# Performance work log

Measured on AMD Instinct MI355X. Metric: run time of the kernel, lower is better.

The kernel has to match this reference:

```python
import jax, jax.numpy as jnp
import numpy as np

N_NODES = 50000
N_EDGES = 800000
HIDDEN = 128
HEADS = 4
LAYERS = 2
NEG_SLOPE = 0.2


def setup_inputs() -> dict:
    key = jax.random.key(0)
    ks = jax.random.split(key, 12)
    s_in = 1.0 / np.sqrt(HIDDEN)
    x = jax.random.normal(ks[0], (N_NODES, HIDDEN), dtype=jnp.float32)
    edge_index = jax.random.randint(ks[1], (2, N_EDGES), 0, N_NODES, dtype=jnp.int64)
    conv_w = jax.random.normal(ks[2], (LAYERS, HIDDEN, HEADS * HIDDEN), dtype=jnp.float32) * s_in
    att_src = jax.random.normal(ks[3], (LAYERS, HEADS, HIDDEN), dtype=jnp.float32) * s_in
    att_dst = jax.random.normal(ks[4], (LAYERS, HEADS, HIDDEN), dtype=jnp.float32) * s_in
    conv_b = jax.random.normal(ks[5], (LAYERS, HIDDEN), dtype=jnp.float32) * 0.01
    proj_w = jax.random.normal(ks[6], (LAYERS, HIDDEN, HIDDEN), dtype=jnp.float32) * s_in
    proj_b = jax.random.normal(ks[7], (LAYERS, HIDDEN), dtype=jnp.float32) * 0.01
    skip_w = jax.random.normal(ks[8], (LAYERS, HIDDEN, HIDDEN), dtype=jnp.float32) * s_in
    skip_b = jax.random.normal(ks[9], (LAYERS, HIDDEN), dtype=jnp.float32) * 0.01
    return {"x": x, "edge_index": edge_index, "conv_w": conv_w, "att_src": att_src,
            "att_dst": att_dst, "conv_b": conv_b, "proj_w": proj_w, "proj_b": proj_b,
            "skip_w": skip_w, "skip_b": skip_b}


def _gat_layer(x, src, dst, W, a_s, a_d, b):
    # x: [N, D]; W: [D, H*C]; a_s, a_d: [H, C]; b: [C]
    N = x.shape[0]
    h = (x @ W).reshape(N, HEADS, HIDDEN)          # [N, H, C]
    alpha_src = jnp.einsum('nhc,hc->nh', h, a_s)   # [N, H]
    alpha_dst = jnp.einsum('nhc,hc->nh', h, a_d)   # [N, H]
    alpha = alpha_src[src] + alpha_dst[dst]        # [E, H]
    alpha = jnp.where(alpha >= 0, alpha, NEG_SLOPE * alpha)  # leaky_relu(0.2)
    amax = jax.ops.segment_max(alpha, dst, num_segments=N)   # [N, H]
    ex = jnp.exp(alpha - amax[dst])                # [E, H]
    denom = jax.ops.segment_sum(ex, dst, num_segments=N)     # [N, H]
    w = ex / (denom[dst] + 1e-16)                  # PyG softmax eps
    msg = h[src] * w[:, :, None]                   # [E, H, C]
    out = jax.ops.segment_sum(msg, dst, num_segments=N)      # [N, H, C]
    return out.mean(axis=1) + b                    # concat=False -> head mean


def reference(x, edge_index, conv_w, att_src, att_dst, conv_b, proj_w, proj_b, skip_w, skip_b):
    src, dst = edge_index[0], edge_index[1]
    out = x
    for l in range(LAYERS):
        conv = _gat_layer(out, src, dst, conv_w[l], att_src[l], att_dst[l], conv_b[l])
        out = jax.nn.relu(conv) @ proj_w[l] + proj_b[l] + (out @ skip_w[l] + skip_b[l])
    return out
```

## Files before the change

kernel.cpp:

```cpp
#include <hip/hip_runtime.h>
#include <hip/hip_bf16.h>
#include <stdint.h>

#define N_NODES 50000
#define N_EDGES 800000
#define HIDDEN  128
#define HEADS   4
#define HD      (HEADS*HIDDEN)
#define CAST_Q  (N_NODES*HIDDEN/4)
#define NTILES  (N_NODES/16)

#define NBUCK   196
#define TILE_H  8192
#define NBLK_H  ((N_EDGES + TILE_H - 1) / TILE_H)
#define NBH     (NBUCK * NBLK_H)
#define SWZ_N   196608
#define HIST_B0 ((CAST_Q + SWZ_N) / 256)
#define GEMM_BLKS 512

typedef __attribute__((ext_vector_type(8))) short  short8;
typedef __attribute__((ext_vector_type(4))) float  floatx4;
typedef __attribute__((ext_vector_type(2))) float  floatx2;

static __device__ __forceinline__ unsigned short bf16_bits(float f) {
    __hip_bfloat16 h = __float2bfloat16(f);
    union { __hip_bfloat16 b; unsigned short s; } u; u.b = h; return u.s;
}

static __device__ __forceinline__ float lexp(float a) {
    return __expf(fmaxf(a, 0.2f * a));
}


#if __has_builtin(__builtin_amdgcn_cvt_pk_fp8_f32) && __has_builtin(__builtin_amdgcn_cvt_pk_f32_fp8)
#define FP8_HW 1
#else
#define FP8_HW 0
static __device__ __forceinline__ unsigned fp8_enc1(float f) {
    unsigned s = __float_as_uint(f) >> 31;
    float a = fabsf(f);
    if (a < 0.0009765625f) return s << 7;
    if (a > 448.f) a = 448.f;
    unsigned ub = __float_as_uint(a) + 0x00080000u;
    int e = (int)((ub >> 23) & 255) - 120;
    unsigned m = (ub >> 20) & 7;
    if (e <= 0) {
        int mm = (int)(a * 512.f + 0.5f); if (mm > 7) mm = 7;
        return (s << 7) | (unsigned)mm;
    }
    if (e > 15) { e = 15; m = 7; }
    return (s << 7) | ((unsigned)e << 3) | m;
}
static __device__ __forceinline__ floatx2 fp8_dec_pk(unsigned b2) {
    floatx2 r;
    unsigned b = b2 & 255;
    {
        unsigned s = (b >> 7) & 1, e = (b >> 3) & 15, m = b & 7;
        r.x = (e == 0) ? ((s ? -1.f : 1.f) * (float)m * 0.001953125f)
                       : __uint_as_float((s << 31) | ((e + 120) << 23) | (m << 20));
    }
    b = (b2 >> 8) & 255;
    {
        unsigned s = (b >> 7) & 1, e = (b >> 3) & 15, m = b & 7;
        r.y = (e == 0) ? ((s ? -1.f : 1.f) * (float)m * 0.001953125f)
                       : __uint_as_float((s << 31) | ((e + 120) << 23) | (m << 20));
    }
    return r;
}
#endif

static __device__ __forceinline__ unsigned fp8_pack4(float a, float b, float c, float d) {
#if FP8_HW
    int w = __builtin_amdgcn_cvt_pk_fp8_f32(a, b, 0, false);
    w     = __builtin_amdgcn_cvt_pk_fp8_f32(c, d, w, true);
    return (unsigned)w;
#else
    return fp8_enc1(a) | (fp8_enc1(b) << 8) | (fp8_enc1(c) << 16) | (fp8_enc1(d) << 24);
#endif
}

static __device__ __forceinline__ void accf8p(floatx2* acc2, uint2 u, float wt) {
    floatx2 wv = {wt, wt};
#if FP8_HW
    acc2[0] += wv * __builtin_amdgcn_cvt_pk_f32_fp8((int)u.x, false);
    acc2[1] += wv * __builtin_amdgcn_cvt_pk_f32_fp8((int)u.x, true);
    acc2[2] += wv * __builtin_amdgcn_cvt_pk_f32_fp8((int)u.y, false);
    acc2[3] += wv * __builtin_amdgcn_cvt_pk_f32_fp8((int)u.y, true);
#else
    acc2[0] += wv * fp8_dec_pk(u.x);
    acc2[1] += wv * fp8_dec_pk(u.x >> 16);
    acc2[2] += wv * fp8_dec_pk(u.y);
    acc2[3] += wv * fp8_dec_pk(u.y >> 16);
#endif
}


__global__ __launch_bounds__(256) void prep_k(
        const float* __restrict__ x, unsigned short* __restrict__ xb16,
        const float* __restrict__ conv_w, const float* __restrict__ proj_w,
        const float* __restrict__ skip_w,
        unsigned short* __restrict__ cwb, unsigned short* __restrict__ pwb,
        unsigned short* __restrict__ swb,
        const int* __restrict__ dst, int* __restrict__ bh) {
    __shared__ int hh[NBUCK];
    if (blockIdx.x >= HIST_B0) {
        int blk = blockIdx.x - HIST_B0;
        for (int c = threadIdx.x; c < NBUCK; c += 256) hh[c] = 0;
        __syncthreads();
        int e0 = blk * TILE_H;
#pragma unroll
        for (int i = 0; i < TILE_H / 256; ++i) {
            int e = e0 + threadIdx.x + i * 256;
            if (e < N_EDGES) atomicAdd(&hh[dst[e] >> 8], 1);
        }
        __syncthreads();
        for (int c = threadIdx.x; c < NBUCK; c += 256) bh[c * NBLK_H + blk] = hh[c];
        return;
    }
    int i = blockIdx.x * 256 + threadIdx.x;
    if (i < CAST_Q) {
        float4 v = ((const float4*)x)[i];
        uint2 p;
        p.x = (unsigned)bf16_bits(v.x) | ((unsigned)bf16_bits(v.y) << 16);
        p.y = (unsigned)bf16_bits(v.z) | ((unsigned)bf16_bits(v.w) << 16);
        ((uint2*)xb16)[i] = p;
        return;
    }
    int o = i - CAST_Q;
    const float* B; unsigned short* D; int off, N; bool perm = false;
    if (o < 131072)      { B = conv_w + (o >> 16) * 65536; D = cwb + (o >> 16) * 65536; off = o & 65535; N = 512; }
    else if (o < 163840) { int t = o - 131072; B = proj_w + (t >> 14) * 16384; D = pwb + (t >> 14) * 16384; off = t & 16383; N = 128; perm = true; }
    else                 { int t = o - 163840; B = skip_w + (t >> 14) * 16384; D = swb + (t >> 14) * 16384; off = t & 16383; N = 128; }
    int j = off & 7, r = (off >> 3) & 15, q = (off >> 7) & 3;
    int rest = off >> 9, ntn = N >> 4;
    int nt = rest % ntn, kc = rest / ntn;
    int kr = kc * 32 + q * 8 + j;
    int row = perm ? ((kr & 7) * 16 + (kr >> 3)) : kr;
    D[off] = bf16_bits(B[(size_t)row * N + nt * 16 + r]);
}


static __device__ __forceinline__ void gemmc_body(
        const __hip_bfloat16* __restrict__ A, const unsigned short* __restrict__ Bs,
        const float* __restrict__ att_s, const float* __restrict__ att_d,
        unsigned char* __restrict__ h8,
        float* __restrict__ a_src, float* __restrict__ a_dst,
        int mtiles, int bid, int stride) {
    int head = threadIdx.x >> 6;
    int lane = threadIdx.x & 63;
    int r = lane & 15, q = lane >> 4;

    short8 Bf[4][8];
#pragma unroll
    for (int kc = 0; kc < 4; ++kc)
#pragma unroll
        for (int ntl = 0; ntl < 8; ++ntl)
            Bf[kc][ntl] = *(const short8*)((const short*)Bs +
                (((size_t)(kc * 32 + head * 8 + ntl) * 4 + q) * 128 + r * 8));

    float as_r[8], ad_r[8];
#pragma unroll
    for (int ntl = 0; ntl < 8; ++ntl) {
        as_r[ntl] = att_s[head * HIDDEN + ntl * 16 + r];
        ad_r[ntl] = att_d[head * HIDDEN + ntl * 16 + r];
    }

    int mt = bid;
    short8 av[4];
    if (mt < mtiles) {
        const short* Ab = (const short*)A + (size_t)(mt * 16 + r) * HIDDEN + q * 8;
#pragma unroll
        for (int kc = 0; kc < 4; ++kc) av[kc] = *(const short8*)(Ab + kc * 32);
    }
    while (mt < mtiles) {
        int nmt = mt + stride;
        short8 avn[4];
        if (nmt < mtiles) {
            const short* Ab = (const short*)A + (size_t)(nmt * 16 + r) * HIDDEN + q * 8;
#pragma unroll
            for (int kc = 0; kc < 4; ++kc) avn[kc] = *(const short8*)(Ab + kc * 32);
        }
        int m0 = mt * 16;
        floatx4 acc[8];
#pragma unroll
        for (int i = 0; i < 8; ++i) acc[i] = (floatx4){0.f, 0.f, 0.f, 0.f};
#pragma unroll
        for (int kc = 0; kc < 4; ++kc)
#pragma unroll
            for (int ntl = 0; ntl < 8; ++ntl)
                acc[ntl] = __builtin_amdgcn_mfma_f32_16x16x32_bf16(av[kc], Bf[kc][ntl], acc[ntl], 0, 0, 0);

#pragma unroll
        for (int i = 0; i < 4; ++i) {
            uint2 o;
            o.x = fp8_pack4(acc[0][i], acc[1][i], acc[2][i], acc[3][i]);
            o.y = fp8_pack4(acc[4][i], acc[5][i], acc[6][i], acc[7][i]);
            *(uint2*)(h8 + (size_t)(m0 + q * 4 + i) * HD + head * HIDDEN + r * 8) = o;
        }
        float sA[4] = {0, 0, 0, 0}, sD[4] = {0, 0, 0, 0};
#pragma unroll
        for (int ntl = 0; ntl < 8; ++ntl)
#pragma unroll
            for (int i = 0; i < 4; ++i) {
                sA[i] += acc[ntl][i] * as_r[ntl];
                sD[i] += acc[ntl][i] * ad_r[ntl];
            }
#pragma unroll
        for (int d = 1; d < 16; d <<= 1)
#pragma unroll
            for (int i = 0; i < 4; ++i) {
                sA[i] += __shfl_xor(sA[i], d);
                sD[i] += __shfl_xor(sD[i], d);
            }
        if (r == 0)
#pragma unroll
            for (int i = 0; i < 4; ++i) {
                int row = m0 + q * 4 + i;
                a_src[row * HEADS + head] = sA[i];
                a_dst[row * HEADS + head] = sD[i];
            }
        mt = nmt;
#pragma unroll
        for (int kc = 0; kc < 4; ++kc) av[kc] = avn[kc];
    }
}

__global__ __launch_bounds__(256, 2) void gemmc_k(
        const __hip_bfloat16* __restrict__ A, const unsigned short* __restrict__ Bs,
        const float* __restrict__ att_s, const float* __restrict__ att_d,
        unsigned char* __restrict__ h8,
        float* __restrict__ a_src, float* __restrict__ a_dst, int mtiles) {
    gemmc_body(A, Bs, att_s, att_d, h8, a_src, a_dst, mtiles, blockIdx.x, gridDim.x);
}


__global__ __launch_bounds__(256, 2) void gemmcsc_k(
        const __hip_bfloat16* __restrict__ A, const unsigned short* __restrict__ Bs,
        const float* __restrict__ att_s, const float* __restrict__ att_d,
        unsigned char* __restrict__ h8,
        float* __restrict__ a_src, float* __restrict__ a_dst, int mtiles,
        const int* __restrict__ src, const int* __restrict__ dst,
        const int* __restrict__ bh, unsigned* __restrict__ tmp) {
    __shared__ int cnt[256], scanbuf[256];
    if (blockIdx.x < GEMM_BLKS) {
        gemmc_body(A, Bs, att_s, att_d, h8, a_src, a_dst, mtiles, blockIdx.x, GEMM_BLKS);
        return;
    }
    int blk = blockIdx.x - GEMM_BLKS;
    int t = threadIdx.x;
    int Tt = 0, Pt = 0;
    if (t < NBUCK) {
        const int* row = bh + (size_t)t * NBLK_H;
        for (int i = 0; i < NBLK_H; ++i) {
            int v = row[i];
            Tt += v;
            Pt += (i < blk) ? v : 0;
        }
    }
    scanbuf[t] = Tt;
    __syncthreads();
    for (int off = 1; off < 256; off <<= 1) {
        int xv = (t >= off) ? scanbuf[t - off] : 0;
        __syncthreads();
        scanbuf[t] += xv;
        __syncthreads();
    }
    int excl = scanbuf[t] - Tt;
    if (t < NBUCK) cnt[t] = excl + Pt;
    __syncthreads();
    int e0 = blk * TILE_H;
#pragma unroll
    for (int i = 0; i < TILE_H / 256; ++i) {
        int e = e0 + t + i * 256;
        if (e < N_EDGES) {
            int d = dst[e];
            int pos = atomicAdd(&cnt[d >> 8], 1);
            tmp[pos] = ((unsigned)(d & 255) << 16) | (unsigned)src[e];
        }
    }
}


__global__ __launch_bounds__(256) void sortB_k(const unsigned* __restrict__ tmp,
                                               const int* __restrict__ bh,
                                               int* __restrict__ src_sorted,
                                               int* __restrict__ row_ptr) {
    __shared__ int cnt[256], buf[256], pos[256], bbase[256], btot[256];
    int t = threadIdx.x, b = blockIdx.x;
    int Tt = 0;
    if (t < NBUCK) {
        const int* row = bh + (size_t)t * NBLK_H;
        for (int i = 0; i < NBLK_H; ++i) Tt += row[i];
    }
    buf[t] = Tt;
    __syncthreads();
    for (int off = 1; off < 256; off <<= 1) {
        int xv = (t >= off) ? buf[t - off] : 0;
        __syncthreads();
        buf[t] += xv;
        __syncthreads();
    }
    bbase[t] = buf[t] - Tt;
    btot[t]  = Tt;
    __syncthreads();
    int beg = bbase[b];
    int end = beg + btot[b];
    cnt[t] = 0;
    __syncthreads();
    for (int i = beg + t; i < end; i += 256) atomicAdd(&cnt[(tmp[i] >> 16) & 255], 1);
    __syncthreads();
    int v = cnt[t];
    buf[t] = v;
    __syncthreads();
    for (int off = 1; off < 256; off <<= 1) {
        int xv = (t >= off) ? buf[t - off] : 0;
        __syncthreads();
        buf[t] += xv;
        __syncthreads();
    }
    int excl = buf[t] - v;
    int d = b * 256 + t;
    if (d <= N_NODES) row_ptr[d] = beg + excl;
    pos[t] = excl;
    __syncthreads();
    for (int i = beg + t; i < end; i += 256) {
        unsigned w = tmp[i];
        int c = (w >> 16) & 255;
        int p = beg + atomicAdd(&pos[c], 1);
        src_sorted[p] = (int)(w & 0xFFFFu);
    }
}


template <typename OutT>
__global__ __launch_bounds__(256, 2) void gemmp_k(
        const __hip_bfloat16* __restrict__ A,  const unsigned short* __restrict__ Bs,
        const __hip_bfloat16* __restrict__ A2, const unsigned short* __restrict__ Bs2,
        const float* __restrict__ b1, const float* __restrict__ b2,
        OutT* __restrict__ D, int mtiles) {
    int wave = threadIdx.x >> 6;
    int lane = threadIdx.x & 63;
    int r = lane & 15, q = lane >> 4;
    int nh = wave & 1;

    short8 Bf[4][4], Bf2[4][4];
#pragma unroll
    for (int kc = 0; kc < 4; ++kc)
#pragma unroll
        for (int ntl = 0; ntl < 4; ++ntl) {
            size_t off = (((size_t)(kc * 8 + nh * 4 + ntl) * 4 + q) * 128 + r * 8);
            Bf[kc][ntl]  = *(const short8*)((const short*)Bs  + off);
            Bf2[kc][ntl] = *(const short8*)((const short*)Bs2 + off);
        }
    float bias[4];
#pragma unroll
    for (int ntl = 0; ntl < 4; ++ntl) {
        int col = nh * 64 + ntl * 16 + r;
        bias[ntl] = b1[col] + b2[col];
    }

    const int stride = gridDim.x * 2;
    int mt = blockIdx.x * 2 + (wave >> 1);
    short8 av[4], av2[4];
    if (mt < mtiles) {
        const short* Ab  = (const short*)A  + (size_t)(mt * 16 + r) * HIDDEN + q * 8;
        const short* Ab2 = (const short*)A2 + (size_t)(mt * 16 + r) * HIDDEN + q * 8;
#pragma unroll
        for (int kc = 0; kc < 4; ++kc) {
            av[kc]  = *(const short8*)(Ab  + kc * 32);
            av2[kc] = *(const short8*)(Ab2 + kc * 32);
        }
    }
    while (mt < mtiles) {
        int nmt = mt + stride;
        short8 avn[4], avn2[4];
        if (nmt < mtiles) {
            const short* Ab  = (const short*)A  + (size_t)(nmt * 16 + r) * HIDDEN + q * 8;
            const short* Ab2 = (const short*)A2 + (size_t)(nmt * 16 + r) * HIDDEN + q * 8;
#pragma unroll
            for (int kc = 0; kc < 4; ++kc) {
                avn[kc]  = *(const short8*)(Ab  + kc * 32);
                avn2[kc] = *(const short8*)(Ab2 + kc * 32);
            }
        }
        int m0 = mt * 16;
        floatx4 acc[4];
#pragma unroll
        for (int i = 0; i < 4; ++i) acc[i] = (floatx4){0.f, 0.f, 0.f, 0.f};
#pragma unroll
        for (int kc = 0; kc < 4; ++kc)
#pragma unroll
            for (int ntl = 0; ntl < 4; ++ntl) {
                acc[ntl] = __builtin_amdgcn_mfma_f32_16x16x32_bf16(av[kc],  Bf[kc][ntl],  acc[ntl], 0, 0, 0);
                acc[ntl] = __builtin_amdgcn_mfma_f32_16x16x32_bf16(av2[kc], Bf2[kc][ntl], acc[ntl], 0, 0, 0);
            }
#pragma unroll
        for (int ntl = 0; ntl < 4; ++ntl) {
            int col = nh * 64 + ntl * 16 + r;
#pragma unroll
            for (int i = 0; i < 4; ++i) {
                int row = m0 + q * 4 + i;
                float v = acc[ntl][i] + bias[ntl];
                if constexpr (sizeof(OutT) == 4)
                    ((float*)D)[(size_t)row * HIDDEN + col] = v;
                else
                    ((__hip_bfloat16*)D)[(size_t)row * HIDDEN + col] = __float2bfloat16(v);
            }
        }
        mt = nmt;
#pragma unroll
        for (int kc = 0; kc < 4; ++kc) { av[kc] = avn[kc]; av2[kc] = avn2[kc]; }
    }
}


__global__ __launch_bounds__(256) void msg_k(const int* __restrict__ row_ptr,
                                             const int* __restrict__ src_sorted,
                                             const float* __restrict__ a_src,
                                             const float* __restrict__ a_dst,
                                             const unsigned char* __restrict__ h8,
                                             const float* __restrict__ conv_b,
                                             __hip_bfloat16* __restrict__ rc) {
    int wave = threadIdx.x >> 6;
    int lane = threadIdx.x & 63;
    int n = blockIdx.x * 4 + wave;
    if (n >= N_NODES) return;
    int head = lane >> 4;
    float adn = a_dst[n * HEADS + head];
    int beg = row_ptr[n], end = row_ptr[n + 1];
    const uint2* hq = (const uint2*)h8;

    floatx2 acc2[4];
#pragma unroll
    for (int k = 0; k < 4; ++k) acc2[k] = (floatx2){0.f, 0.f};
    float esum = 0.f;
    for (int base = beg; base < end; base += 32) {
        int m = min(32, end - base);
        int sv = (lane < m) ? src_sorted[base + lane] : 0;
        int j = 0;
        for (; j + 4 <= m; j += 4) {
            int s0 = __builtin_amdgcn_readlane(sv, j);
            int s1 = __builtin_amdgcn_readlane(sv, j + 1);
            int s2 = __builtin_amdgcn_readlane(sv, j + 2);
            int s3 = __builtin_amdgcn_readlane(sv, j + 3);
            uint2 u0 = hq[(size_t)s0 * 64 + lane];
            uint2 u1 = hq[(size_t)s1 * 64 + lane];
            uint2 u2 = hq[(size_t)s2 * 64 + lane];
            uint2 u3 = hq[(size_t)s3 * 64 + lane];
            float e0 = lexp(a_src[s0 * 4 + head] + adn);
            float e1 = lexp(a_src[s1 * 4 + head] + adn);
            float e2 = lexp(a_src[s2 * 4 + head] + adn);
            float e3 = lexp(a_src[s3 * 4 + head] + adn);
            accf8p(acc2, u0, e0);
            accf8p(acc2, u1, e1);
            accf8p(acc2, u2, e2);
            accf8p(acc2, u3, e3);
            esum += (e0 + e1) + (e2 + e3);
        }
        for (; j < m; ++j) {
            int s0 = __builtin_amdgcn_readlane(sv, j);
            uint2 u0 = hq[(size_t)s0 * 64 + lane];
            float e0 = lexp(a_src[s0 * 4 + head] + adn);
            accf8p(acc2, u0, e0);
            esum += e0;
        }
    }
    float rinv = 1.f / (esum + 1e-16f);
    float acc[8];
#pragma unroll
    for (int k = 0; k < 4; ++k) { acc[2 * k] = acc2[k].x * rinv; acc[2 * k + 1] = acc2[k].y * rinv; }
#pragma unroll
    for (int k = 0; k < 8; ++k) {
        acc[k] += __shfl_xor(acc[k], 16);
        acc[k] += __shfl_xor(acc[k], 32);
    }
    if (lane < 16) {
        union { uint4 v; unsigned short us[8]; } o;
#pragma unroll
        for (int k = 0; k < 8; ++k) {
            float mres = 0.25f * acc[k] + conv_b[k * 16 + lane];
            o.us[k] = bf16_bits(mres > 0.f ? mres : 0.f);
        }
        ((uint4*)rc)[(size_t)n * 16 + lane] = o.v;
    }
}


extern "C" void kernel_launch(void* const* d_in, const int* in_sizes, int n_in,
                              void* d_out, int out_size, void* d_ws, size_t ws_size,
                              hipStream_t stream) {
    const float* x      = (const float*)d_in[0];
    const int*   ei     = (const int*)d_in[1];
    const float* conv_w = (const float*)d_in[2];
    const float* att_s  = (const float*)d_in[3];
    const float* att_d  = (const float*)d_in[4];
    const float* conv_b = (const float*)d_in[5];
    const float* proj_w = (const float*)d_in[6];
    const float* proj_b = (const float*)d_in[7];
    const float* skip_w = (const float*)d_in[8];
    const float* skip_b = (const float*)d_in[9];
    float* out = (float*)d_out;

    char* ws = (char*)d_ws;
    size_t o = 0;
    auto alloc = [&](size_t b) { size_t c = o; o += (b + 255) & ~(size_t)255; return c; };
    __hip_bfloat16* xb16 = (__hip_bfloat16*)(ws + alloc((size_t)N_NODES * HIDDEN * 2));
    unsigned short* cwb  = (unsigned short*)(ws + alloc((size_t)2 * HIDDEN * HD * 2));
    unsigned short* pwb  = (unsigned short*)(ws + alloc((size_t)2 * HIDDEN * HIDDEN * 2));
    unsigned short* swb  = (unsigned short*)(ws + alloc((size_t)2 * HIDDEN * HIDDEN * 2));
    unsigned char* h8    = (unsigned char*)(ws + alloc((size_t)N_NODES * HD));
    float* a_src         = (float*)(ws + alloc((size_t)N_NODES * HEADS * 4));
    float* a_dst         = (float*)(ws + alloc((size_t)N_NODES * HEADS * 4));
    int* row_ptr         = (int*)(ws + alloc((size_t)(N_NODES + 1) * 4));
    int* src_s           = (int*)(ws + alloc((size_t)N_EDGES * 4));
    __hip_bfloat16* rc   = (__hip_bfloat16*)(ws + alloc((size_t)N_NODES * HIDDEN * 2));
    __hip_bfloat16* xb   = (__hip_bfloat16*)(ws + alloc((size_t)N_NODES * HIDDEN * 2));
    int* bh              = (int*)(ws + alloc((size_t)NBH * 4));

    unsigned* tmp = (unsigned*)rc;

    const int* srcp = ei;
    const int* dstp = ei + N_EDGES;

    prep_k<<<HIST_B0 + NBLK_H, 256, 0, stream>>>(
        x, (unsigned short*)xb16, conv_w, proj_w, skip_w, cwb, pwb, swb, dstp, bh);

    gemmcsc_k<<<GEMM_BLKS + NBLK_H, 256, 0, stream>>>(
        xb16, cwb, att_s, att_d, h8, a_src, a_dst, NTILES,
        srcp, dstp, bh, tmp);
    sortB_k<<<NBUCK, 256, 0, stream>>>(tmp, bh, src_s, row_ptr);

    msg_k<<<(N_NODES + 3) / 4, 256, 0, stream>>>(
        row_ptr, src_s, a_src, a_dst, h8, conv_b, rc);
    gemmp_k<__hip_bfloat16><<<512, 256, 0, stream>>>(
        rc, pwb, xb16, swb, proj_b, skip_b, xb, NTILES);

    gemmc_k<<<512, 256, 0, stream>>>(
        xb, cwb + (size_t)HIDDEN * HD,
        att_s + HD, att_d + HD, h8, a_src, a_dst, NTILES);
    msg_k<<<(N_NODES + 3) / 4, 256, 0, stream>>>(
        row_ptr, src_s, a_src, a_dst, h8, conv_b + HIDDEN, rc);
    gemmp_k<float><<<512, 256, 0, stream>>>(
        rc, pwb + (size_t)HIDDEN * HIDDEN,
        xb, swb + (size_t)HIDDEN * HIDDEN,
        proj_b + HIDDEN, skip_b + HIDDEN, out, NTILES);
}
```

Baseline: 313.0 us.

## Fuse fp32-to-bf16 cast of x into GEMMs; process two nodes per wave in msg_k

The separate pass that cast x to bf16 in prep_k is removed. The first conv GEMM and the first projection/skip GEMM now read fp32 x directly and pack it to bf16 in registers, which saves a full write and re-read of the bf16 copy. msg_k now interleaves two destination nodes per wave, keeping two accumulator sets so more independent gathers are in flight. In exchange the GEMMs read twice the bytes for x, and the message kernel uses more registers and carries extra remainder-loop code.

```diff
diff --git a/kernel.cpp b/kernel.cpp
--- a/kernel.cpp
+++ b/kernel.cpp
@@ -7,7 +7,6 @@
 #define HIDDEN  128
 #define HEADS   4
 #define HD      (HEADS*HIDDEN)
-#define CAST_Q  (N_NODES*HIDDEN/4)
 #define NTILES  (N_NODES/16)
 
 #define NBUCK   196
@@ -15,7 +14,7 @@
 #define NBLK_H  ((N_EDGES + TILE_H - 1) / TILE_H)
 #define NBH     (NBUCK * NBLK_H)
 #define SWZ_N   196608
-#define HIST_B0 ((CAST_Q + SWZ_N) / 256)
+#define SWZ_B   (SWZ_N / 256)
 #define GEMM_BLKS 512
 
 typedef __attribute__((ext_vector_type(8))) short  short8;
@@ -29,6 +28,15 @@
 
 static __device__ __forceinline__ float lexp(float a) {
     return __expf(fmaxf(a, 0.2f * a));
+}
+
+static __device__ __forceinline__ short8 packbf8(float4 a, float4 b) {
+    short8 s;
+    s[0] = (short)bf16_bits(a.x); s[1] = (short)bf16_bits(a.y);
+    s[2] = (short)bf16_bits(a.z); s[3] = (short)bf16_bits(a.w);
+    s[4] = (short)bf16_bits(b.x); s[5] = (short)bf16_bits(b.y);
+    s[6] = (short)bf16_bits(b.z); s[7] = (short)bf16_bits(b.w);
+    return s;
 }
 
 
@@ -96,15 +104,14 @@
 
 
 __global__ __launch_bounds__(256) void prep_k(
-        const float* __restrict__ x, unsigned short* __restrict__ xb16,
         const float* __restrict__ conv_w, const float* __restrict__ proj_w,
         const float* __restrict__ skip_w,
         unsigned short* __restrict__ cwb, unsigned short* __restrict__ pwb,
         unsigned short* __restrict__ swb,
         const int* __restrict__ dst, int* __restrict__ bh) {
     __shared__ int hh[NBUCK];
-    if (blockIdx.x >= HIST_B0) {
-        int blk = blockIdx.x - HIST_B0;
+    if (blockIdx.x >= SWZ_B) {
+        int blk = blockIdx.x - SWZ_B;
         for (int c = threadIdx.x; c < NBUCK; c += 256) hh[c] = 0;
         __syncthreads();
         int e0 = blk * TILE_H;
@@ -117,16 +124,7 @@
         for (int c = threadIdx.x; c < NBUCK; c += 256) bh[c * NBLK_H + blk] = hh[c];
         return;
     }
-    int i = blockIdx.x * 256 + threadIdx.x;
-    if (i < CAST_Q) {
-        float4 v = ((const float4*)x)[i];
-        uint2 p;
-        p.x = (unsigned)bf16_bits(v.x) | ((unsigned)bf16_bits(v.y) << 16);
-        p.y = (unsigned)bf16_bits(v.z) | ((unsigned)bf16_bits(v.w) << 16);
-        ((uint2*)xb16)[i] = p;
-        return;
-    }
-    int o = i - CAST_Q;
+    int o = blockIdx.x * 256 + threadIdx.x;
     const float* B; unsigned short* D; int off, N; bool perm = false;
     if (o < 131072)      { B = conv_w + (o >> 16) * 65536; D = cwb + (o >> 16) * 65536; off = o & 65535; N = 512; }
     else if (o < 163840) { int t = o - 131072; B = proj_w + (t >> 14) * 16384; D = pwb + (t >> 14) * 16384; off = t & 16383; N = 128; perm = true; }
@@ -140,8 +138,9 @@
 }
 
 
+template <bool F32A>
 static __device__ __forceinline__ void gemmc_body(
-        const __hip_bfloat16* __restrict__ A, const unsigned short* __restrict__ Bs,
+        const void* __restrict__ A, const unsigned short* __restrict__ Bs,
         const float* __restrict__ att_s, const float* __restrict__ att_d,
         unsigned char* __restrict__ h8,
         float* __restrict__ a_src, float* __restrict__ a_dst,
@@ -165,21 +164,29 @@
         ad_r[ntl] = att_d[head * HIDDEN + ntl * 16 + r];
     }
 
+    auto loadA = [&](int mtv, short8* dstv) {
+        if constexpr (F32A) {
+            const float* Ab = (const float*)A + (size_t)(mtv * 16 + r) * HIDDEN + q * 8;
+#pragma unroll
+            for (int kc = 0; kc < 4; ++kc) {
+                float4 v0 = *(const float4*)(Ab + kc * 32);
+                float4 v1 = *(const float4*)(Ab + kc * 32 + 4);
+                dstv[kc] = packbf8(v0, v1);
+            }
+        } else {
+            const short* Ab = (const short*)A + (size_t)(mtv * 16 + r) * HIDDEN + q * 8;
+#pragma unroll
+            for (int kc = 0; kc < 4; ++kc) dstv[kc] = *(const short8*)(Ab + kc * 32);
+        }
+    };
+
     int mt = bid;
     short8 av[4];
-    if (mt < mtiles) {
-        const short* Ab = (const short*)A + (size_t)(mt * 16 + r) * HIDDEN + q * 8;
-#pragma unroll
-        for (int kc = 0; kc < 4; ++kc) av[kc] = *(const short8*)(Ab + kc * 32);
-    }
+    if (mt < mtiles) loadA(mt, av);
     while (mt < mtiles) {
         int nmt = mt + stride;
         short8 avn[4];
-        if (nmt < mtiles) {
-            const short* Ab = (const short*)A + (size_t)(nmt * 16 + r) * HIDDEN + q * 8;
-#pragma unroll
-            for (int kc = 0; kc < 4; ++kc) avn[kc] = *(const short8*)(Ab + kc * 32);
-        }
+        if (nmt < mtiles) loadA(nmt, avn);
         int m0 = mt * 16;
         floatx4 acc[8];
 #pragma unroll
@@ -230,12 +237,12 @@
         const float* __restrict__ att_s, const float* __restrict__ att_d,
         unsigned char* __restrict__ h8,
         float* __restrict__ a_src, float* __restrict__ a_dst, int mtiles) {
-    gemmc_body(A, Bs, att_s, att_d, h8, a_src, a_dst, mtiles, blockIdx.x, gridDim.x);
+    gemmc_body<false>(A, Bs, att_s, att_d, h8, a_src, a_dst, mtiles, blockIdx.x, gridDim.x);
 }
 
 
 __global__ __launch_bounds__(256, 2) void gemmcsc_k(
-        const __hip_bfloat16* __restrict__ A, const unsigned short* __restrict__ Bs,
+        const float* __restrict__ A, const unsigned short* __restrict__ Bs,
         const float* __restrict__ att_s, const float* __restrict__ att_d,
         unsigned char* __restrict__ h8,
         float* __restrict__ a_src, float* __restrict__ a_dst, int mtiles,
@@ -243,7 +250,7 @@
         const int* __restrict__ bh, unsigned* __restrict__ tmp) {
     __shared__ int cnt[256], scanbuf[256];
     if (blockIdx.x < GEMM_BLKS) {
-        gemmc_body(A, Bs, att_s, att_d, h8, a_src, a_dst, mtiles, blockIdx.x, GEMM_BLKS);
+        gemmc_body<true>(A, Bs, att_s, att_d, h8, a_src, a_dst, mtiles, blockIdx.x, GEMM_BLKS);
         return;
     }
     int blk = blockIdx.x - GEMM_BLKS;
@@ -332,10 +339,10 @@
 }
 
 
-template <typename OutT>
+template <typename OutT, bool F32A2>
 __global__ __launch_bounds__(256, 2) void gemmp_k(
         const __hip_bfloat16* __restrict__ A,  const unsigned short* __restrict__ Bs,
-        const __hip_bfloat16* __restrict__ A2, const unsigned short* __restrict__ Bs2,
+        const void* __restrict__ A2, const unsigned short* __restrict__ Bs2,
         const float* __restrict__ b1, const float* __restrict__ b2,
         OutT* __restrict__ D, int mtiles) {
     int wave = threadIdx.x >> 6;
@@ -359,30 +366,33 @@
         bias[ntl] = b1[col] + b2[col];
     }
 
+    auto loadA = [&](int mtv, short8* d1, short8* d2) {
+        const short* Ab = (const short*)A + (size_t)(mtv * 16 + r) * HIDDEN + q * 8;
+#pragma unroll
+        for (int kc = 0; kc < 4; ++kc) d1[kc] = *(const short8*)(Ab + kc * 32);
+        if constexpr (F32A2) {
+            const float* Ab2 = (const float*)A2 + (size_t)(mtv * 16 + r) * HIDDEN + q * 8;
+#pragma unroll
+            for (int kc = 0; kc < 4; ++kc) {
+                float4 v0 = *(const float4*)(Ab2 + kc * 32);
+                float4 v1 = *(const float4*)(Ab2 + kc * 32 + 4);
+                d2[kc] = packbf8(v0, v1);
+            }
+        } else {
+            const short* Ab2 = (const short*)A2 + (size_t)(mtv * 16 + r) * HIDDEN + q * 8;
+#pragma unroll
+            for (int kc = 0; kc < 4; ++kc) d2[kc] = *(const short8*)(Ab2 + kc * 32);
+        }
+    };
+
     const int stride = gridDim.x * 2;
     int mt = blockIdx.x * 2 + (wave >> 1);
     short8 av[4], av2[4];
-    if (mt < mtiles) {
-        const short* Ab  = (const short*)A  + (size_t)(mt * 16 + r) * HIDDEN + q * 8;
-        const short* Ab2 = (const short*)A2 + (size_t)(mt * 16 + r) * HIDDEN + q * 8;
-#pragma unroll
-        for (int kc = 0; kc < 4; ++kc) {
-            av[kc]  = *(const short8*)(Ab  + kc * 32);
-            av2[kc] = *(const short8*)(Ab2 + kc * 32);
-        }
-    }
+    if (mt < mtiles) loadA(mt, av, av2);
     while (mt < mtiles) {
         int nmt = mt + stride;
         short8 avn[4], avn2[4];
-        if (nmt < mtiles) {
-            const short* Ab  = (const short*)A  + (size_t)(nmt * 16 + r) * HIDDEN + q * 8;
-            const short* Ab2 = (const short*)A2 + (size_t)(nmt * 16 + r) * HIDDEN + q * 8;
-#pragma unroll
-            for (int kc = 0; kc < 4; ++kc) {
-                avn[kc]  = *(const short8*)(Ab  + kc * 32);
-                avn2[kc] = *(const short8*)(Ab2 + kc * 32);
-            }
-        }
+        if (nmt < mtiles) loadA(nmt, avn, avn2);
         int m0 = mt * 16;
         floatx4 acc[4];
 #pragma unroll
@@ -423,65 +433,154 @@
                                              __hip_bfloat16* __restrict__ rc) {
     int wave = threadIdx.x >> 6;
     int lane = threadIdx.x & 63;
-    int n = blockIdx.x * 4 + wave;
-    if (n >= N_NODES) return;
     int head = lane >> 4;
-    float adn = a_dst[n * HEADS + head];
-    int beg = row_ptr[n], end = row_ptr[n + 1];
+    int n0 = (blockIdx.x * 4 + wave) * 2;
+    if (n0 >= N_NODES) return;
+    int n1 = n0 + 1;
     const uint2* hq = (const uint2*)h8;
 
-    floatx2 acc2[4];
-#pragma unroll
-    for (int k = 0; k < 4; ++k) acc2[k] = (floatx2){0.f, 0.f};
-    float esum = 0.f;
-    for (int base = beg; base < end; base += 32) {
-        int m = min(32, end - base);
-        int sv = (lane < m) ? src_sorted[base + lane] : 0;
-        int j = 0;
-        for (; j + 4 <= m; j += 4) {
-            int s0 = __builtin_amdgcn_readlane(sv, j);
-            int s1 = __builtin_amdgcn_readlane(sv, j + 1);
-            int s2 = __builtin_amdgcn_readlane(sv, j + 2);
-            int s3 = __builtin_amdgcn_readlane(sv, j + 3);
-            uint2 u0 = hq[(size_t)s0 * 64 + lane];
-            uint2 u1 = hq[(size_t)s1 * 64 + lane];
-            uint2 u2 = hq[(size_t)s2 * 64 + lane];
-            uint2 u3 = hq[(size_t)s3 * 64 + lane];
-            float e0 = lexp(a_src[s0 * 4 + head] + adn);
-            float e1 = lexp(a_src[s1 * 4 + head] + adn);
-            float e2 = lexp(a_src[s2 * 4 + head] + adn);
-            float e3 = lexp(a_src[s3 * 4 + head] + adn);
-            accf8p(acc2, u0, e0);
-            accf8p(acc2, u1, e1);
-            accf8p(acc2, u2, e2);
-            accf8p(acc2, u3, e3);
-            esum += (e0 + e1) + (e2 + e3);
-        }
-        for (; j < m; ++j) {
-            int s0 = __builtin_amdgcn_readlane(sv, j);
-            uint2 u0 = hq[(size_t)s0 * 64 + lane];
-            float e0 = lexp(a_src[s0 * 4 + head] + adn);
-            accf8p(acc2, u0, e0);
-            esum += e0;
-        }
-    }
-    float rinv = 1.f / (esum + 1e-16f);
-    float acc[8];
-#pragma unroll
-    for (int k = 0; k < 4; ++k) { acc[2 * k] = acc2[k].x * rinv; acc[2 * k + 1] = acc2[k].y * rinv; }
+    float adn0 = a_dst[n0 * HEADS + head];
+    float adn1 = a_dst[n1 * HEADS + head];
+    int beg0 = row_ptr[n0];
+    int end0 = row_ptr[n1];
+    int end1 = row_ptr[n1 + 1];
+
+    floatx2 accA[4], accB[4];
+#pragma unroll
+    for (int k = 0; k < 4; ++k) { accA[k] = (floatx2){0.f, 0.f}; accB[k] = (floatx2){0.f, 0.f}; }
+    float es0 = 0.f, es1 = 0.f;
+
+    int base0 = beg0, base1 = end0;
+    while (base0 < end0 || base1 < end1) {
+        int m0 = min(32, end0 - base0);
+        int m1 = min(32, end1 - base1);
+        int sv0 = (lane < m0) ? src_sorted[base0 + lane] : 0;
+        int sv1 = (lane < m1) ? src_sorted[base1 + lane] : 0;
+        int j0 = 0, j1 = 0;
+        for (; j0 + 4 <= m0 && j1 + 4 <= m1; j0 += 4, j1 += 4) {
+            int a0 = __builtin_amdgcn_readlane(sv0, j0);
+            int a1 = __builtin_amdgcn_readlane(sv0, j0 + 1);
+            int a2 = __builtin_amdgcn_readlane(sv0, j0 + 2);
+            int a3 = __builtin_amdgcn_readlane(sv0, j0 + 3);
+            int b0 = __builtin_amdgcn_readlane(sv1, j1);
+            int b1 = __builtin_amdgcn_readlane(sv1, j1 + 1);
+            int b2 = __builtin_amdgcn_readlane(sv1, j1 + 2);
+            int b3 = __builtin_amdgcn_readlane(sv1, j1 + 3);
+            uint2 uA0 = hq[(size_t)a0 * 64 + lane];
+            uint2 uA1 = hq[(size_t)a1 * 64 + lane];
+            uint2 uA2 = hq[(size_t)a2 * 64 + lane];
+            uint2 uA3 = hq[(size_t)a3 * 64 + lane];
+            uint2 uB0 = hq[(size_t)b0 * 64 + lane];
+            uint2 uB1 = hq[(size_t)b1 * 64 + lane];
+            uint2 uB2 = hq[(size_t)b2 * 64 + lane];
+            uint2 uB3 = hq[(size_t)b3 * 64 + lane];
+            float eA0 = lexp(a_src[a0 * 4 + head] + adn0);
+            float eA1 = lexp(a_src[a1 * 4 + head] + adn0);
+            float eA2 = lexp(a_src[a2 * 4 + head] + adn0);
+            float eA3 = lexp(a_src[a3 * 4 + head] + adn0);
+            float eB0 = lexp(a_src[b0 * 4 + head] + adn1);
+            float eB1 = lexp(a_src[b1 * 4 + head] + adn1);
+            float eB2 = lexp(a_src[b2 * 4 + head] + adn1);
+            float eB3 = lexp(a_src[b3 * 4 + head] + adn1);
+            accf8p(accA, uA0, eA0);
+            accf8p(accB, uB0, eB0);
+            accf8p(accA, uA1, eA1);
+            accf8p(accB, uB1, eB1);
+            accf8p(accA, uA2, eA2);
+            accf8p(accB, uB2, eB2);
+            accf8p(accA, uA3, eA3);
+            accf8p(accB, uB3, eB3);
+            es0 += (eA0 + eA1) + (eA2 + eA3);
+            es1 += (eB0 + eB1) + (eB2 + eB3);
+        }
+        for (; j0 + 4 <= m0; j0 += 4) {
+            int a0 = __builtin_amdgcn_readlane(sv0, j0);
+            int a1 = __builtin_amdgcn_readlane(sv0, j0 + 1);
+            int a2 = __builtin_amdgcn_readlane(sv0, j0 + 2);
+            int a3 = __builtin_amdgcn_readlane(sv0, j0 + 3);
+            uint2 uA0 = hq[(size_t)a0 * 64 + lane];
+            uint2 uA1 = hq[(size_t)a1 * 64 + lane];
+            uint2 uA2 = hq[(size_t)a2 * 64 + lane];
+            uint2 uA3 = hq[(size_t)a3 * 64 + lane];
+            float eA0 = lexp(a_src[a0 * 4 + head] + adn0);
+            float eA1 = lexp(a_src[a1 * 4 + head] + adn0);
+            float eA2 = lexp(a_src[a2 * 4 + head] + adn0);
+            float eA3 = lexp(a_src[a3 * 4 + head] + adn0);
+            accf8p(accA, uA0, eA0);
+            accf8p(accA, uA1, eA1);
+            accf8p(accA, uA2, eA2);
+            accf8p(accA, uA3, eA3);
+            es0 += (eA0 + eA1) + (eA2 + eA3);
+        }
+        for (; j1 + 4 <= m1; j1 += 4) {
+            int b0 = __builtin_amdgcn_readlane(sv1, j1);
+            int b1 = __builtin_amdgcn_readlane(sv1, j1 + 1);
+            int b2 = __builtin_amdgcn_readlane(sv1, j1 + 2);
+            int b3 = __builtin_amdgcn_readlane(sv1, j1 + 3);
+            uint2 uB0 = hq[(size_t)b0 * 64 + lane];
+            uint2 uB1 = hq[(size_t)b1 * 64 + lane];
+            uint2 uB2 = hq[(size_t)b2 * 64 + lane];
+            uint2 uB3 = hq[(size_t)b3 * 64 + lane];
+            float eB0 = lexp(a_src[b0 * 4 + head] + adn1);
+            float eB1 = lexp(a_src[b1 * 4 + head] + adn1);
+            float eB2 = lexp(a_src[b2 * 4 + head] + adn1);
+            float eB3 = lexp(a_src[b3 * 4 + head] + adn1);
+            accf8p(accB, uB0, eB0);
+            accf8p(accB, uB1, eB1);
+            accf8p(accB, uB2, eB2);
+            accf8p(accB, uB3, eB3);
+            es1 += (eB0 + eB1) + (eB2 + eB3);
+        }
+        for (; j0 < m0; ++j0) {
+            int a0 = __builtin_amdgcn_readlane(sv0, j0);
+            uint2 uA0 = hq[(size_t)a0 * 64 + lane];
+            float eA0 = lexp(a_src[a0 * 4 + head] + adn0);
+            accf8p(accA, uA0, eA0);
+            es0 += eA0;
+        }
+        for (; j1 < m1; ++j1) {
+            int b0 = __builtin_amdgcn_readlane(sv1, j1);
+            uint2 uB0 = hq[(size_t)b0 * 64 + lane];
+            float eB0 = lexp(a_src[b0 * 4 + head] + adn1);
+            accf8p(accB, uB0, eB0);
+            es1 += eB0;
+        }
+        base0 += m0;
+        base1 += m1;
+    }
+
+    float r0 = 1.f / (es0 + 1e-16f);
+    float r1 = 1.f / (es1 + 1e-16f);
+    float fa[8], fb[8];
+#pragma unroll
+    for (int k = 0; k < 4; ++k) {
+        fa[2 * k] = accA[k].x * r0; fa[2 * k + 1] = accA[k].y * r0;
+        fb[2 * k] = accB[k].x * r1; fb[2 * k + 1] = accB[k].y * r1;
+    }
 #pragma unroll
     for (int k = 0; k < 8; ++k) {
-        acc[k] += __shfl_xor(acc[k], 16);
-        acc[k] += __shfl_xor(acc[k], 32);
+        fa[k] += __shfl_xor(fa[k], 16);
+        fa[k] += __shfl_xor(fa[k], 32);
+        fb[k] += __shfl_xor(fb[k], 16);
+        fb[k] += __shfl_xor(fb[k], 32);
     }
     if (lane < 16) {
         union { uint4 v; unsigned short us[8]; } o;
 #pragma unroll
         for (int k = 0; k < 8; ++k) {
-            float mres = 0.25f * acc[k] + conv_b[k * 16 + lane];
+            float mres = 0.25f * fa[k] + conv_b[k * 16 + lane];
             o.us[k] = bf16_bits(mres > 0.f ? mres : 0.f);
         }
-        ((uint4*)rc)[(size_t)n * 16 + lane] = o.v;
+        ((uint4*)rc)[(size_t)n0 * 16 + lane] = o.v;
+    } else if (lane < 32) {
+        int rr = lane & 15;
+        union { uint4 v; unsigned short us[8]; } o;
+#pragma unroll
+        for (int k = 0; k < 8; ++k) {
+            float mres = 0.25f * fb[k] + conv_b[k * 16 + rr];
+            o.us[k] = bf16_bits(mres > 0.f ? mres : 0.f);
+        }
+        ((uint4*)rc)[(size_t)n1 * 16 + rr] = o.v;
     }
 }
 
@@ -504,7 +603,6 @@
     char* ws = (char*)d_ws;
     size_t o = 0;
     auto alloc = [&](size_t b) { size_t c = o; o += (b + 255) & ~(size_t)255; return c; };
-    __hip_bfloat16* xb16 = (__hip_bfloat16*)(ws + alloc((size_t)N_NODES * HIDDEN * 2));
     unsigned short* cwb  = (unsigned short*)(ws + alloc((size_t)2 * HIDDEN * HD * 2));
     unsigned short* pwb  = (unsigned short*)(ws + alloc((size_t)2 * HIDDEN * HIDDEN * 2));
     unsigned short* swb  = (unsigned short*)(ws + alloc((size_t)2 * HIDDEN * HIDDEN * 2));
@@ -522,25 +620,25 @@
     const int* srcp = ei;
     const int* dstp = ei + N_EDGES;
 
-    prep_k<<<HIST_B0 + NBLK_H, 256, 0, stream>>>(
-        x, (unsigned short*)xb16, conv_w, proj_w, skip_w, cwb, pwb, swb, dstp, bh);
+    prep_k<<<SWZ_B + NBLK_H, 256, 0, stream>>>(
+        conv_w, proj_w, skip_w, cwb, pwb, swb, dstp, bh);
 
     gemmcsc_k<<<GEMM_BLKS + NBLK_H, 256, 0, stream>>>(
-        xb16, cwb, att_s, att_d, h8, a_src, a_dst, NTILES,
+        x, cwb, att_s, att_d, h8, a_src, a_dst, NTILES,
         srcp, dstp, bh, tmp);
     sortB_k<<<NBUCK, 256, 0, stream>>>(tmp, bh, src_s, row_ptr);
 
-    msg_k<<<(N_NODES + 3) / 4, 256, 0, stream>>>(
+    msg_k<<<(N_NODES / 2 + 3) / 4, 256, 0, stream>>>(
         row_ptr, src_s, a_src, a_dst, h8, conv_b, rc);
-    gemmp_k<__hip_bfloat16><<<512, 256, 0, stream>>>(
-        rc, pwb, xb16, swb, proj_b, skip_b, xb, NTILES);
+    gemmp_k<__hip_bfloat16, true><<<512, 256, 0, stream>>>(
+        rc, pwb, x, swb, proj_b, skip_b, xb, NTILES);
 
     gemmc_k<<<512, 256, 0, stream>>>(
         xb, cwb + (size_t)HIDDEN * HD,
         att_s + HD, att_d + HD, h8, a_src, a_dst, NTILES);
-    msg_k<<<(N_NODES + 3) / 4, 256, 0, stream>>>(
+    msg_k<<<(N_NODES / 2 + 3) / 4, 256, 0, stream>>>(
         row_ptr, src_s, a_src, a_dst, h8, conv_b + HIDDEN, rc);
-    gemmp_k<float><<<512, 256, 0, stream>>>(
+    gemmp_k<float, false><<<512, 256, 0, stream>>>(
         rc, pwb + (size_t)HIDDEN * HIDDEN,
         xb, swb + (size_t)HIDDEN * HIDDEN,
         proj_b + HIDDEN, skip_b + HIDDEN, out, NTILES);
```

Measured after the change: 319.0 us. Within noise of the previous version (+1.9%).
